# Kernel tuning notes

Hardware: AMD Instinct MI355X
Metric: run time of the kernel (lower is better)

Reference implementation:

```python
import jax, jax.numpy as jnp
import numpy as np

N = 100_000
E = 1_000_000
F_IN = 128
F_OUT = 64
NHOP = 2


def _xavier(k, shape, gain=1.414):
    fan_in, fan_out = shape
    std = gain * np.sqrt(2.0 / (fan_in + fan_out))
    return (jax.random.normal(k, shape) * std).astype(jnp.float32)


def setup_inputs() -> dict:
    key = jax.random.key(0)
    ks = jax.random.split(key, 8)
    x = jax.random.normal(ks[0], (N, F_IN), jnp.float32)
    edge_index = jax.random.randint(ks[1], (2, E), 0, N)
    edge_attr = jax.random.uniform(ks[2], (E,), jnp.float32)
    W0 = _xavier(ks[3], (F_IN, F_OUT))
    W1 = _xavier(ks[4], (F_IN, F_OUT))
    b0 = jnp.zeros((F_OUT,), jnp.float32)
    b1 = jnp.zeros((F_OUT,), jnp.float32)
    fc0 = _xavier(ks[5], (F_OUT, 1))
    fc1 = _xavier(ks[6], (F_OUT, 1))
    bf0 = jnp.zeros((1,), jnp.float32)
    bf1 = jnp.zeros((1,), jnp.float32)
    return dict(x=x, edge_index=edge_index, edge_attr=edge_attr,
                W0=W0, b0=b0, W1=W1, b1=b1,
                fc0=fc0, bf0=bf0, fc1=fc1, bf1=bf1)


def _spmm(row, col, val, v, n):
    # (A v)[r] = sum over edges (r -> c) of val * v[c]
    return jax.ops.segment_sum(val[:, None] * v[col], row, num_segments=n)


def _adaptive_enc(y, fc, bf):
    # NodeAdaptiveEncoder (eval mode): relu(y) + sigmoid(y@fc+bf) * min(y, 0)
    g = jax.nn.sigmoid(y @ fc + bf)  # [N, 1]
    return jnp.where(y < 0, 0.0, y) + g * jnp.where(y > 0, 0.0, y)


def reference(x, edge_index, edge_attr, W0, b0, W1, b1, fc0, bf0, fc1, bf1):
    n = x.shape[0]
    row, col = edge_index[0], edge_index[1]
    ones = jnp.ones((n, 1), x.dtype)
    params = [(W0, b0, fc0, bf0), (W1, b1, fc1, bf1)]
    outs = []
    for hop in range(NHOP):
        W, b, fc, bf = params[hop]
        h = x @ W  # [N, F_OUT]
        # identity attention; row_uniform norm of A^(hop+1) factors as
        # (A^(hop+1) h) / (A^(hop+1) 1) -- exact since spspmm sums duplicates.
        agg, deg = h, ones
        for _ in range(hop + 1):
            agg = _spmm(row, col, edge_attr, agg, n)
            deg = _spmm(row, col, edge_attr, deg, n)
        safe_deg = jnp.where(deg > 0, deg, 1.0)
        y = jnp.where(deg > 0, agg / safe_deg, 0.0)  # NaN mask for empty rows
        y = y + b
        outs.append(_adaptive_enc(y, fc, bf))
    return jnp.concatenate(outs, axis=1)  # [N, NHOP * F_OUT]
```

## Files before the change

### kernel.cpp

```cpp
#include <hip/hip_runtime.h>

#define F_IN 128
#define F_ALL 128
#define F_HOP 64

#define RPB_BITS 9
#define RPB 512
#define KB_MAX 256
#define NBLK_BIN 256
#define ECAP 6144

typedef unsigned int uint;
typedef unsigned short ushort;
typedef __attribute__((ext_vector_type(8))) short short8v;
typedef __attribute__((ext_vector_type(4))) float float4v;

__device__ __forceinline__ uint pack_bf16(float lo, float hi) {
    uint ul = __float_as_uint(lo), uh = __float_as_uint(hi);
    ul += 0x7FFFu + ((ul >> 16) & 1u);
    uh += 0x7FFFu + ((uh >> 16) & 1u);
    return (ul >> 16) | (uh & 0xFFFF0000u);
}
__device__ __forceinline__ float bf_lo(uint h) { return __uint_as_float(h << 16); }
__device__ __forceinline__ float bf_hi(uint h) { return __uint_as_float(h & 0xFFFF0000u); }

__global__ __launch_bounds__(256) void gemm_mfma_kernel(
    const float* __restrict__ x, const float* __restrict__ W0,
    const float* __restrict__ W1, uint* __restrict__ H2, int N) {
    __shared__ ushort Wlds[16384];

    {
        const int t = threadIdx.x;
        #pragma unroll
        for (int i = 0; i < 8; ++i) {
            const int e    = t + 256 * i;
            const int lane = e & 63;
            const int tile = e >> 6;
            const int kt   = tile >> 3;
            const int nt   = tile & 7;
            const int k0   = kt * 32 + (lane >> 4) * 8;
            const int n    = nt * 16 + (lane & 15);
            const float* src = (n < 64) ? (W0 + n) : (W1 + (n - 64));
            float v[8];
            #pragma unroll
            for (int j = 0; j < 8; ++j) v[j] = src[(size_t)(k0 + j) * F_HOP];
            uint4 o;
            o.x = pack_bf16(v[0], v[1]);
            o.y = pack_bf16(v[2], v[3]);
            o.z = pack_bf16(v[4], v[5]);
            o.w = pack_bf16(v[6], v[7]);
            *((uint4*)Wlds + e) = o;
        }
    }
    __syncthreads();

    const int wv   = threadIdx.x >> 6;
    const int lane = threadIdx.x & 63;
    const int rbase = blockIdx.x * 64 + wv * 16;
    if (rbase >= N) return;

    const int m    = lane & 15;
    const int quad = lane >> 4;
    const float* xrow = x + (size_t)(rbase + m) * F_IN + quad * 8;

    float4v acc[8];
    #pragma unroll
    for (int t = 0; t < 8; ++t) acc[t] = (float4v){0.f, 0.f, 0.f, 0.f};

    #pragma unroll
    for (int kt = 0; kt < 4; ++kt) {
        const float4v xa = __builtin_nontemporal_load((const float4v*)(xrow + kt * 32));
        const float4v xb = __builtin_nontemporal_load((const float4v*)(xrow + kt * 32 + 4));
        union { uint4 u; short8v s; } av;
        av.u.x = pack_bf16(xa[0], xa[1]);
        av.u.y = pack_bf16(xa[2], xa[3]);
        av.u.z = pack_bf16(xb[0], xb[1]);
        av.u.w = pack_bf16(xb[2], xb[3]);
        #pragma unroll
        for (int nt = 0; nt < 8; ++nt) {
            union { uint4 u; short8v s; } bv;
            bv.u = *((const uint4*)Wlds + (kt * 8 + nt) * 64 + lane);
            acc[nt] = __builtin_amdgcn_mfma_f32_16x16x32_bf16(av.s, bv.s, acc[nt], 0, 0, 0);
        }
    }

    #pragma unroll
    for (int t = 0; t < 4; ++t) {
        #pragma unroll
        for (int i = 0; i < 4; ++i) {
            const int r = rbase + quad * 4 + i;
            H2[(size_t)r * F_HOP + t * 16 + m] = pack_bf16(acc[t][i], acc[t + 4][i]);
        }
    }
}

__global__ __launch_bounds__(256) void bucket_hist_kernel(
    const int* __restrict__ ei, int* __restrict__ bhist, int E, int K) {
    __shared__ int h[KB_MAX];
    for (int i = threadIdx.x; i < K; i += 256) h[i] = 0;
    __syncthreads();
    const int chunk = (E + NBLK_BIN - 1) / NBLK_BIN;
    const int s = blockIdx.x * chunk;
    const int e = min(s + chunk, E);
    for (int j = s + threadIdx.x; j < e; j += 256)
        atomicAdd(&h[__builtin_nontemporal_load(ei + j) >> RPB_BITS], 1);
    __syncthreads();
    for (int i = threadIdx.x; i < K; i += 256)
        bhist[blockIdx.x * KB_MAX + i] = h[i];
}

__global__ __launch_bounds__(256) void blockscan_kernel(
    int* __restrict__ bhist, int* __restrict__ btot) {
    __shared__ int wsum[4];
    const int b = blockIdx.x;
    const int t = threadIdx.x;
    const int s = bhist[t * KB_MAX + b];
    int v = s;
    #pragma unroll
    for (int d = 1; d < 64; d <<= 1) {
        int u = __shfl_up(v, (unsigned)d, 64);
        if ((t & 63) >= d) v += u;
    }
    if ((t & 63) == 63) wsum[t >> 6] = v;
    __syncthreads();
    int off = 0;
    #pragma unroll
    for (int i = 0; i < 4; ++i) if (i < (t >> 6)) off += wsum[i];
    bhist[t * KB_MAX + b] = off + v - s;
    if (t == 255) btot[b] = off + v;
}

__global__ __launch_bounds__(256) void total_scan_kernel(
    const int* __restrict__ btot, int* __restrict__ bbase,
    int* __restrict__ rowptr, int E, int K, int N) {
    __shared__ int wsum[4];
    const int t = threadIdx.x;
    const int s = (t < K) ? btot[t] : 0;
    int v = s;
    #pragma unroll
    for (int d = 1; d < 64; d <<= 1) {
        int u = __shfl_up(v, (unsigned)d, 64);
        if ((t & 63) >= d) v += u;
    }
    if ((t & 63) == 63) wsum[t >> 6] = v;
    __syncthreads();
    int off = 0;
    #pragma unroll
    for (int i = 0; i < 4; ++i) if (i < (t >> 6)) off += wsum[i];
    const int excl = off + v - s;
    if (t < K) bbase[t] = excl;
    if (t == 0) { bbase[K] = E; rowptr[N] = E; }
}

__global__ __launch_bounds__(256) void bin_kernel(
    const int* __restrict__ ei, const float* __restrict__ ea,
    const int* __restrict__ bloc, const int* __restrict__ bbase,
    int2* __restrict__ gbuf, int E, int K) {
    __shared__ int cur[KB_MAX];
    for (int i = threadIdx.x; i < K; i += 256)
        cur[i] = bbase[i] + bloc[blockIdx.x * KB_MAX + i];
    __syncthreads();
    const int chunk = (E + NBLK_BIN - 1) / NBLK_BIN;
    const int s0 = blockIdx.x * chunk;
    const int e0 = min(s0 + chunk, E);
    for (int j = s0 + threadIdx.x; j < e0; j += 256) {
        const int r = __builtin_nontemporal_load(ei + j);
        const int c = __builtin_nontemporal_load(ei + E + j);
        const int vv = __float_as_int(__builtin_nontemporal_load(ea + j));
        const int b = r >> RPB_BITS;
        const int gp = atomicAdd(&cur[b], 1);
        gbuf[gp] = make_int2(c | ((r & (RPB - 1)) << 17), vv);
    }
}

__global__ __launch_bounds__(1024) void sort_kernel(
    const int* __restrict__ bbase, const int2* __restrict__ gbuf,
    int2* __restrict__ ecv, int* __restrict__ rowptr, int N) {
    __shared__ int2 ebuf[ECAP];
    __shared__ int cnt[RPB];
    __shared__ int wsum[8];
    const int b = blockIdx.x;
    const int t = threadIdx.x;
    const int bstart = bbase[b], bend = bbase[b + 1];
    const int m = bend - bstart;
    const int row0 = b << RPB_BITS;
    if (t < RPB) cnt[t] = 0;
    __syncthreads();
    for (int j = t; j < m; j += 1024) {
        const int2 p = gbuf[bstart + j];
        if (j < ECAP) ebuf[j] = p;
        atomicAdd(&cnt[(p.x >> 17) & (RPB - 1)], 1);
    }
    __syncthreads();
    int v = 0, s = 0;
    if (t < RPB) {
        s = cnt[t];
        v = s;
        #pragma unroll
        for (int d = 1; d < 64; d <<= 1) {
            int u = __shfl_up(v, (unsigned)d, 64);
            if ((t & 63) >= d) v += u;
        }
        if ((t & 63) == 63) wsum[t >> 6] = v;
    }
    __syncthreads();
    if (t < RPB) {
        int off = 0;
        #pragma unroll
        for (int i = 0; i < 8; ++i) if (i < (t >> 6)) off += wsum[i];
        const int excl = off + v - s;
        const int r0 = row0 + t;
        if (r0 < N) rowptr[r0] = bstart + excl;
        cnt[t] = excl;
    }
    __syncthreads();
    for (int j = t; j < m; j += 1024) {
        const int2 p = (j < ECAP) ? ebuf[j] : gbuf[bstart + j];
        const int lr = (p.x >> 17) & (RPB - 1);
        const int pos = atomicAdd(&cnt[lr], 1);
        ecv[bstart + pos] = make_int2(p.x & 0x1FFFF, p.y);
    }
}

__global__ __launch_bounds__(256) void pass1_kernel(
    const int* __restrict__ rowptr, const int2* __restrict__ ecv,
    const uint* __restrict__ H2,
    const float* __restrict__ b0, const float* __restrict__ fc0,
    const float* __restrict__ bf0,
    float* __restrict__ out, ushort* __restrict__ T16,
    float* __restrict__ dg1, int N) {
    const int lane = threadIdx.x & 63;
    const int g    = lane >> 4;
    const int l    = lane & 15;
    const int r = blockIdx.x * 16 + (threadIdx.x >> 6) * 4 + g;
    if (r >= N) return;
    const int f0 = l * 4;
    const uint* __restrict__ H2b = H2 + f0;
    const int jb = rowptr[r], je = rowptr[r + 1];

    float s00 = 0.f, s01 = 0.f, s02 = 0.f, s03 = 0.f;
    float s10 = 0.f, s11 = 0.f, s12 = 0.f, s13 = 0.f;
    float d = 0.f;
    int j = jb;
    for (; j + 4 <= je; j += 4) {
        const int2 e0 = ecv[j], e1 = ecv[j + 1], e2 = ecv[j + 2], e3 = ecv[j + 3];
        const uint4 h0 = *(const uint4*)(H2b + (size_t)e0.x * F_HOP);
        const uint4 h1 = *(const uint4*)(H2b + (size_t)e1.x * F_HOP);
        const uint4 h2 = *(const uint4*)(H2b + (size_t)e2.x * F_HOP);
        const uint4 h3 = *(const uint4*)(H2b + (size_t)e3.x * F_HOP);
        const float v0 = __int_as_float(e0.y), v1 = __int_as_float(e1.y);
        const float v2 = __int_as_float(e2.y), v3 = __int_as_float(e3.y);
        d += (v0 + v1) + (v2 + v3);
        s00 = fmaf(v0, bf_lo(h0.x), s00); s10 = fmaf(v0, bf_hi(h0.x), s10);
        s01 = fmaf(v0, bf_lo(h0.y), s01); s11 = fmaf(v0, bf_hi(h0.y), s11);
        s02 = fmaf(v0, bf_lo(h0.z), s02); s12 = fmaf(v0, bf_hi(h0.z), s12);
        s03 = fmaf(v0, bf_lo(h0.w), s03); s13 = fmaf(v0, bf_hi(h0.w), s13);
        s00 = fmaf(v1, bf_lo(h1.x), s00); s10 = fmaf(v1, bf_hi(h1.x), s10);
        s01 = fmaf(v1, bf_lo(h1.y), s01); s11 = fmaf(v1, bf_hi(h1.y), s11);
        s02 = fmaf(v1, bf_lo(h1.z), s02); s12 = fmaf(v1, bf_hi(h1.z), s12);
        s03 = fmaf(v1, bf_lo(h1.w), s03); s13 = fmaf(v1, bf_hi(h1.w), s13);
        s00 = fmaf(v2, bf_lo(h2.x), s00); s10 = fmaf(v2, bf_hi(h2.x), s10);
        s01 = fmaf(v2, bf_lo(h2.y), s01); s11 = fmaf(v2, bf_hi(h2.y), s11);
        s02 = fmaf(v2, bf_lo(h2.z), s02); s12 = fmaf(v2, bf_hi(h2.z), s12);
        s03 = fmaf(v2, bf_lo(h2.w), s03); s13 = fmaf(v2, bf_hi(h2.w), s13);
        s00 = fmaf(v3, bf_lo(h3.x), s00); s10 = fmaf(v3, bf_hi(h3.x), s10);
        s01 = fmaf(v3, bf_lo(h3.y), s01); s11 = fmaf(v3, bf_hi(h3.y), s11);
        s02 = fmaf(v3, bf_lo(h3.z), s02); s12 = fmaf(v3, bf_hi(h3.z), s12);
        s03 = fmaf(v3, bf_lo(h3.w), s03); s13 = fmaf(v3, bf_hi(h3.w), s13);
    }
    for (; j < je; ++j) {
        const int2 e0 = ecv[j];
        const uint4 h0 = *(const uint4*)(H2b + (size_t)e0.x * F_HOP);
        const float v0 = __int_as_float(e0.y);
        d += v0;
        s00 = fmaf(v0, bf_lo(h0.x), s00); s10 = fmaf(v0, bf_hi(h0.x), s10);
        s01 = fmaf(v0, bf_lo(h0.y), s01); s11 = fmaf(v0, bf_hi(h0.y), s11);
        s02 = fmaf(v0, bf_lo(h0.z), s02); s12 = fmaf(v0, bf_hi(h0.z), s12);
        s03 = fmaf(v0, bf_lo(h0.w), s03); s13 = fmaf(v0, bf_hi(h0.w), s13);
    }

    uint2 tw;
    tw.x = pack_bf16(s10, s11);
    tw.y = pack_bf16(s12, s13);
    *(uint2*)(T16 + (size_t)r * F_HOP + f0) = tw;
    if (l == 0) dg1[r] = d;

    const float inv = (d > 0.f) ? 1.f / d : 0.f;
    const float4 bb = *(const float4*)(b0 + f0);
    const float4 ff = *(const float4*)(fc0 + f0);
    const float y0 = s00 * inv + bb.x;
    const float y1 = s01 * inv + bb.y;
    const float y2 = s02 * inv + bb.z;
    const float y3 = s03 * inv + bb.w;
    float t = y0 * ff.x + y1 * ff.y + y2 * ff.z + y3 * ff.w;
    #pragma unroll
    for (int m = 1; m < 16; m <<= 1) t += __shfl_xor(t, m, 64);
    const float gg = 1.f / (1.f + __expf(-(t + bf0[0])));
    float4v o;
    o[0] = fmaxf(y0, 0.f) + gg * fminf(y0, 0.f);
    o[1] = fmaxf(y1, 0.f) + gg * fminf(y1, 0.f);
    o[2] = fmaxf(y2, 0.f) + gg * fminf(y2, 0.f);
    o[3] = fmaxf(y3, 0.f) + gg * fminf(y3, 0.f);
    __builtin_nontemporal_store(o, (float4v*)(out + (size_t)r * F_ALL + f0));
}

__global__ __launch_bounds__(256) void pass2_kernel(
    const int* __restrict__ rowptr, const int2* __restrict__ ecv,
    const ushort* __restrict__ T16, const float* __restrict__ dg1,
    const float* __restrict__ b1, const float* __restrict__ fc1,
    const float* __restrict__ bf1,
    float* __restrict__ out, int N) {
    const int lane = threadIdx.x & 63;
    const int g    = lane >> 4;
    const int l    = lane & 15;
    const int r = blockIdx.x * 16 + (threadIdx.x >> 6) * 4 + g;
    if (r >= N) return;
    const int f0 = l * 4;
    const ushort* __restrict__ Tb = T16 + f0;
    const int jb = rowptr[r], je = rowptr[r + 1];

    float s0 = 0.f, s1 = 0.f, s2 = 0.f, s3 = 0.f;
    float d2 = 0.f;
    int j = jb;
    for (; j + 4 <= je; j += 4) {
        const int2 e0 = ecv[j], e1 = ecv[j + 1], e2 = ecv[j + 2], e3 = ecv[j + 3];
        const uint2 t0 = *(const uint2*)(Tb + (size_t)e0.x * F_HOP);
        const uint2 t1 = *(const uint2*)(Tb + (size_t)e1.x * F_HOP);
        const uint2 t2 = *(const uint2*)(Tb + (size_t)e2.x * F_HOP);
        const uint2 t3 = *(const uint2*)(Tb + (size_t)e3.x * F_HOP);
        const float g0 = dg1[e0.x], g1 = dg1[e1.x], g2 = dg1[e2.x], g3 = dg1[e3.x];
        const float v0 = __int_as_float(e0.y), v1 = __int_as_float(e1.y);
        const float v2 = __int_as_float(e2.y), v3 = __int_as_float(e3.y);
        d2 = fmaf(v0, g0, d2); d2 = fmaf(v1, g1, d2);
        d2 = fmaf(v2, g2, d2); d2 = fmaf(v3, g3, d2);
        s0 = fmaf(v0, bf_lo(t0.x), s0); s1 = fmaf(v0, bf_hi(t0.x), s1);
        s2 = fmaf(v0, bf_lo(t0.y), s2); s3 = fmaf(v0, bf_hi(t0.y), s3);
        s0 = fmaf(v1, bf_lo(t1.x), s0); s1 = fmaf(v1, bf_hi(t1.x), s1);
        s2 = fmaf(v1, bf_lo(t1.y), s2); s3 = fmaf(v1, bf_hi(t1.y), s3);
        s0 = fmaf(v2, bf_lo(t2.x), s0); s1 = fmaf(v2, bf_hi(t2.x), s1);
        s2 = fmaf(v2, bf_lo(t2.y), s2); s3 = fmaf(v2, bf_hi(t2.y), s3);
        s0 = fmaf(v3, bf_lo(t3.x), s0); s1 = fmaf(v3, bf_hi(t3.x), s1);
        s2 = fmaf(v3, bf_lo(t3.y), s2); s3 = fmaf(v3, bf_hi(t3.y), s3);
    }
    for (; j < je; ++j) {
        const int2 e0 = ecv[j];
        const uint2 t0 = *(const uint2*)(Tb + (size_t)e0.x * F_HOP);
        const float v0 = __int_as_float(e0.y);
        d2 = fmaf(v0, dg1[e0.x], d2);
        s0 = fmaf(v0, bf_lo(t0.x), s0); s1 = fmaf(v0, bf_hi(t0.x), s1);
        s2 = fmaf(v0, bf_lo(t0.y), s2); s3 = fmaf(v0, bf_hi(t0.y), s3);
    }

    const float inv = (d2 > 0.f) ? 1.f / d2 : 0.f;
    const float4 bb = *(const float4*)(b1 + f0);
    const float4 ff = *(const float4*)(fc1 + f0);
    const float y0 = s0 * inv + bb.x;
    const float y1 = s1 * inv + bb.y;
    const float y2 = s2 * inv + bb.z;
    const float y3 = s3 * inv + bb.w;
    float t = y0 * ff.x + y1 * ff.y + y2 * ff.z + y3 * ff.w;
    #pragma unroll
    for (int m = 1; m < 16; m <<= 1) t += __shfl_xor(t, m, 64);
    const float gg = 1.f / (1.f + __expf(-(t + bf1[0])));
    float4v o;
    o[0] = fmaxf(y0, 0.f) + gg * fminf(y0, 0.f);
    o[1] = fmaxf(y1, 0.f) + gg * fminf(y1, 0.f);
    o[2] = fmaxf(y2, 0.f) + gg * fminf(y2, 0.f);
    o[3] = fmaxf(y3, 0.f) + gg * fminf(y3, 0.f);
    __builtin_nontemporal_store(o, (float4v*)(out + (size_t)r * F_ALL + F_HOP + f0));
}

extern "C" void kernel_launch(void* const* d_in, const int* in_sizes, int n_in,
                              void* d_out, int out_size, void* d_ws, size_t ws_size,
                              hipStream_t stream) {
    const float* x   = (const float*)d_in[0];
    const int*   ei  = (const int*)  d_in[1];
    const float* ea  = (const float*)d_in[2];
    const float* W0  = (const float*)d_in[3];
    const float* b0  = (const float*)d_in[4];
    const float* W1  = (const float*)d_in[5];
    const float* b1  = (const float*)d_in[6];
    const float* fc0 = (const float*)d_in[7];
    const float* bf0 = (const float*)d_in[8];
    const float* fc1 = (const float*)d_in[9];
    const float* bf1 = (const float*)d_in[10];
    float* out = (float*)d_out;

    const int N = in_sizes[0] / F_IN;
    const int E = in_sizes[2];
    const int K = (N + RPB - 1) >> RPB_BITS;

    uint*   H2   = (uint*)d_ws;
    ushort* T16  = (ushort*)(H2 + (size_t)N * F_HOP);
    float*  dg1  = (float*)(T16 + (size_t)N * F_HOP);
    int2*   gbuf = (int2*)(dg1 + (size_t)((N + 3) & ~3));
    int2*   ecv  = gbuf + (size_t)E;
    int*    bhist = (int*)(ecv + (size_t)E);
    int*    bbase = bhist + (size_t)NBLK_BIN * KB_MAX;
    int*    btot  = bbase + (KB_MAX + 4);
    int*    rowptr = btot + KB_MAX;

    gemm_mfma_kernel<<<(N + 63) / 64, 256, 0, stream>>>(x, W0, W1, H2, N);

    bucket_hist_kernel<<<NBLK_BIN, 256, 0, stream>>>(ei, bhist, E, K);
    blockscan_kernel<<<K, 256, 0, stream>>>(bhist, btot);
    total_scan_kernel<<<1, 256, 0, stream>>>(btot, bbase, rowptr, E, K, N);
    bin_kernel<<<NBLK_BIN, 256, 0, stream>>>(ei, ea, bhist, bbase, gbuf, E, K);
    sort_kernel<<<K, 1024, 0, stream>>>(bbase, gbuf, ecv, rowptr, N);

    pass1_kernel<<<(N + 15) / 16, 256, 0, stream>>>(
        rowptr, ecv, H2, b0, fc0, bf0, out, T16, dg1, N);

    pass2_kernel<<<(N + 15) / 16, 256, 0, stream>>>(
        rowptr, ecv, T16, dg1, b1, fc1, bf1, out, N);
}
```

Measured before the change: 239.2 us.

## Fuse histogram into GEMM launch, fold total scan into bin/sort, shrink buckets

Runs the edge bucket histogram as extra blocks of the GEMM launch, so both share one grid and can overlap. The separate total-scan kernel is removed: bin_kernel and sort_kernel each recompute the bucket base offsets from btot redundantly. Bucket size drops from 512 to 256 rows, which gives more, smaller sort blocks of 512 threads with a smaller shared edge buffer. This cuts two launches and raises sort parallelism, at the cost of redundant scan work per block and more gbuf spill when a bucket exceeds ECAP.

```diff
diff --git a/kernel.cpp b/kernel.cpp
--- a/kernel.cpp
+++ b/kernel.cpp
@@ -4,11 +4,11 @@
 #define F_ALL 128
 #define F_HOP 64
 
-#define RPB_BITS 9
-#define RPB 512
-#define KB_MAX 256
+#define RPB_BITS 8
+#define RPB 256
+#define KB_MAX 512
 #define NBLK_BIN 256
-#define ECAP 6144
+#define ECAP 3072
 
 typedef unsigned int uint;
 typedef unsigned short ushort;
@@ -24,10 +24,28 @@
 __device__ __forceinline__ float bf_lo(uint h) { return __uint_as_float(h << 16); }
 __device__ __forceinline__ float bf_hi(uint h) { return __uint_as_float(h & 0xFFFF0000u); }
 
-__global__ __launch_bounds__(256) void gemm_mfma_kernel(
+__global__ __launch_bounds__(256) void gemm_hist_kernel(
     const float* __restrict__ x, const float* __restrict__ W0,
-    const float* __restrict__ W1, uint* __restrict__ H2, int N) {
+    const float* __restrict__ W1, uint* __restrict__ H2,
+    const int* __restrict__ ei, int* __restrict__ bhist,
+    int N, int E, int K, int gemmBlocks) {
     __shared__ ushort Wlds[16384];
+
+    if ((int)blockIdx.x >= gemmBlocks) {
+        int* h = (int*)Wlds;
+        const int hb = blockIdx.x - gemmBlocks;
+        for (int i = threadIdx.x; i < K; i += 256) h[i] = 0;
+        __syncthreads();
+        const int chunk = (E + NBLK_BIN - 1) / NBLK_BIN;
+        const int s = hb * chunk;
+        const int e = min(s + chunk, E);
+        for (int j = s + threadIdx.x; j < e; j += 256)
+            atomicAdd(&h[__builtin_nontemporal_load(ei + j) >> RPB_BITS], 1);
+        __syncthreads();
+        for (int i = threadIdx.x; i < K; i += 256)
+            bhist[hb * KB_MAX + i] = h[i];
+        return;
+    }
 
     {
         const int t = threadIdx.x;
@@ -94,23 +112,9 @@
     }
 }
 
-__global__ __launch_bounds__(256) void bucket_hist_kernel(
-    const int* __restrict__ ei, int* __restrict__ bhist, int E, int K) {
-    __shared__ int h[KB_MAX];
-    for (int i = threadIdx.x; i < K; i += 256) h[i] = 0;
-    __syncthreads();
-    const int chunk = (E + NBLK_BIN - 1) / NBLK_BIN;
-    const int s = blockIdx.x * chunk;
-    const int e = min(s + chunk, E);
-    for (int j = s + threadIdx.x; j < e; j += 256)
-        atomicAdd(&h[__builtin_nontemporal_load(ei + j) >> RPB_BITS], 1);
-    __syncthreads();
-    for (int i = threadIdx.x; i < K; i += 256)
-        bhist[blockIdx.x * KB_MAX + i] = h[i];
-}
-
 __global__ __launch_bounds__(256) void blockscan_kernel(
-    int* __restrict__ bhist, int* __restrict__ btot) {
+    int* __restrict__ bhist, int* __restrict__ btot,
+    int* __restrict__ rowptr, int E, int N) {
     __shared__ int wsum[4];
     const int b = blockIdx.x;
     const int t = threadIdx.x;
@@ -128,14 +132,21 @@
     for (int i = 0; i < 4; ++i) if (i < (t >> 6)) off += wsum[i];
     bhist[t * KB_MAX + b] = off + v - s;
     if (t == 255) btot[b] = off + v;
-}
-
-__global__ __launch_bounds__(256) void total_scan_kernel(
-    const int* __restrict__ btot, int* __restrict__ bbase,
-    int* __restrict__ rowptr, int E, int K, int N) {
+    if (b == 0 && t == 0) rowptr[N] = E;
+}
+
+__global__ __launch_bounds__(256) void bin_kernel(
+    const int* __restrict__ ei, const float* __restrict__ ea,
+    const int* __restrict__ bloc, const int* __restrict__ btot,
+    int2* __restrict__ gbuf, int E, int K) {
+    __shared__ int bb[KB_MAX];
+    __shared__ int cur[KB_MAX];
     __shared__ int wsum[4];
     const int t = threadIdx.x;
-    const int s = (t < K) ? btot[t] : 0;
+    const int i0 = 2 * t, i1 = 2 * t + 1;
+    const int c0 = (i0 < K) ? btot[i0] : 0;
+    const int c1 = (i1 < K) ? btot[i1] : 0;
+    const int s = c0 + c1;
     int v = s;
     #pragma unroll
     for (int d = 1; d < 64; d <<= 1) {
@@ -144,26 +155,22 @@
     }
     if ((t & 63) == 63) wsum[t >> 6] = v;
     __syncthreads();
-    int off = 0;
-    #pragma unroll
-    for (int i = 0; i < 4; ++i) if (i < (t >> 6)) off += wsum[i];
-    const int excl = off + v - s;
-    if (t < K) bbase[t] = excl;
-    if (t == 0) { bbase[K] = E; rowptr[N] = E; }
-}
-
-__global__ __launch_bounds__(256) void bin_kernel(
-    const int* __restrict__ ei, const float* __restrict__ ea,
-    const int* __restrict__ bloc, const int* __restrict__ bbase,
-    int2* __restrict__ gbuf, int E, int K) {
-    __shared__ int cur[KB_MAX];
-    for (int i = threadIdx.x; i < K; i += 256)
-        cur[i] = bbase[i] + bloc[blockIdx.x * KB_MAX + i];
+    {
+        int off = 0;
+        #pragma unroll
+        for (int i = 0; i < 4; ++i) if (i < (t >> 6)) off += wsum[i];
+        const int excl = off + v - s;
+        if (i0 < K) bb[i0] = excl;
+        if (i1 < K) bb[i1] = excl + c0;
+    }
+    __syncthreads();
+    for (int i = t; i < K; i += 256)
+        cur[i] = bb[i] + bloc[blockIdx.x * KB_MAX + i];
     __syncthreads();
     const int chunk = (E + NBLK_BIN - 1) / NBLK_BIN;
     const int s0 = blockIdx.x * chunk;
     const int e0 = min(s0 + chunk, E);
-    for (int j = s0 + threadIdx.x; j < e0; j += 256) {
+    for (int j = s0 + t; j < e0; j += 256) {
         const int r = __builtin_nontemporal_load(ei + j);
         const int c = __builtin_nontemporal_load(ei + E + j);
         const int vv = __float_as_int(__builtin_nontemporal_load(ea + j));
@@ -173,48 +180,69 @@
     }
 }
 
-__global__ __launch_bounds__(1024) void sort_kernel(
-    const int* __restrict__ bbase, const int2* __restrict__ gbuf,
-    int2* __restrict__ ecv, int* __restrict__ rowptr, int N) {
+__global__ __launch_bounds__(512) void sort_kernel(
+    const int* __restrict__ btot, const int2* __restrict__ gbuf,
+    int2* __restrict__ ecv, int* __restrict__ rowptr, int E, int K, int N) {
     __shared__ int2 ebuf[ECAP];
     __shared__ int cnt[RPB];
-    __shared__ int wsum[8];
+    __shared__ int bb[KB_MAX + 1];
+    __shared__ int wsum[4];
     const int b = blockIdx.x;
     const int t = threadIdx.x;
-    const int bstart = bbase[b], bend = bbase[b + 1];
+    const int i0 = 2 * t, i1 = 2 * t + 1;
+    const int c0 = (t < 256 && i0 < K) ? btot[i0] : 0;
+    const int c1 = (t < 256 && i1 < K) ? btot[i1] : 0;
+    const int s = c0 + c1;
+    int v = s;
+    #pragma unroll
+    for (int d = 1; d < 64; d <<= 1) {
+        int u = __shfl_up(v, (unsigned)d, 64);
+        if ((t & 63) >= d) v += u;
+    }
+    if (t < 256 && (t & 63) == 63) wsum[t >> 6] = v;
+    if (t < RPB) cnt[t] = 0;
+    __syncthreads();
+    if (t < 256) {
+        int off = 0;
+        #pragma unroll
+        for (int i = 0; i < 4; ++i) if (i < (t >> 6)) off += wsum[i];
+        const int excl = off + v - s;
+        if (i0 < K) bb[i0] = excl;
+        if (i1 < K) bb[i1] = excl + c0;
+    }
+    if (t == 0) bb[K] = E;
+    __syncthreads();
+    const int bstart = bb[b], bend = bb[b + 1];
     const int m = bend - bstart;
     const int row0 = b << RPB_BITS;
-    if (t < RPB) cnt[t] = 0;
-    __syncthreads();
-    for (int j = t; j < m; j += 1024) {
+    for (int j = t; j < m; j += 512) {
         const int2 p = gbuf[bstart + j];
         if (j < ECAP) ebuf[j] = p;
         atomicAdd(&cnt[(p.x >> 17) & (RPB - 1)], 1);
     }
     __syncthreads();
-    int v = 0, s = 0;
-    if (t < RPB) {
-        s = cnt[t];
-        v = s;
-        #pragma unroll
-        for (int d = 1; d < 64; d <<= 1) {
-            int u = __shfl_up(v, (unsigned)d, 64);
-            if ((t & 63) >= d) v += u;
-        }
-        if ((t & 63) == 63) wsum[t >> 6] = v;
-    }
-    __syncthreads();
-    if (t < RPB) {
+    const int s2 = (t < 256) ? cnt[t] : 0;
+    int v2 = s2;
+    #pragma unroll
+    for (int d = 1; d < 64; d <<= 1) {
+        int u = __shfl_up(v2, (unsigned)d, 64);
+        if ((t & 63) >= d) v2 += u;
+    }
+    if (t < 256 && (t & 63) == 63) wsum[t >> 6] = v2;
+    __syncthreads();
+    int excl2 = 0;
+    if (t < 256) {
         int off = 0;
         #pragma unroll
-        for (int i = 0; i < 8; ++i) if (i < (t >> 6)) off += wsum[i];
-        const int excl = off + v - s;
+        for (int i = 0; i < 4; ++i) if (i < (t >> 6)) off += wsum[i];
+        excl2 = off + v2 - s2;
         const int r0 = row0 + t;
-        if (r0 < N) rowptr[r0] = bstart + excl;
-        cnt[t] = excl;
-    }
-    __syncthreads();
-    for (int j = t; j < m; j += 1024) {
+        if (r0 < N) rowptr[r0] = bstart + excl2;
+    }
+    __syncthreads();
+    if (t < 256) cnt[t] = excl2;
+    __syncthreads();
+    for (int j = t; j < m; j += 512) {
         const int2 p = (j < ECAP) ? ebuf[j] : gbuf[bstart + j];
         const int lr = (p.x >> 17) & (RPB - 1);
         const int pos = atomicAdd(&cnt[lr], 1);
@@ -396,17 +424,16 @@
     int2*   gbuf = (int2*)(dg1 + (size_t)((N + 3) & ~3));
     int2*   ecv  = gbuf + (size_t)E;
     int*    bhist = (int*)(ecv + (size_t)E);
-    int*    bbase = bhist + (size_t)NBLK_BIN * KB_MAX;
-    int*    btot  = bbase + (KB_MAX + 4);
-    int*    rowptr = btot + KB_MAX;
-
-    gemm_mfma_kernel<<<(N + 63) / 64, 256, 0, stream>>>(x, W0, W1, H2, N);
-
-    bucket_hist_kernel<<<NBLK_BIN, 256, 0, stream>>>(ei, bhist, E, K);
-    blockscan_kernel<<<K, 256, 0, stream>>>(bhist, btot);
-    total_scan_kernel<<<1, 256, 0, stream>>>(btot, bbase, rowptr, E, K, N);
-    bin_kernel<<<NBLK_BIN, 256, 0, stream>>>(ei, ea, bhist, bbase, gbuf, E, K);
-    sort_kernel<<<K, 1024, 0, stream>>>(bbase, gbuf, ecv, rowptr, N);
+    int*    btot  = bhist + (size_t)NBLK_BIN * KB_MAX;
+    int*    rowptr = btot + (KB_MAX + 4);
+
+    const int gemmBlocks = (N + 63) / 64;
+    gemm_hist_kernel<<<gemmBlocks + NBLK_BIN, 256, 0, stream>>>(
+        x, W0, W1, H2, ei, bhist, N, E, K, gemmBlocks);
+
+    blockscan_kernel<<<K, 256, 0, stream>>>(bhist, btot, rowptr, E, N);
+    bin_kernel<<<NBLK_BIN, 256, 0, stream>>>(ei, ea, bhist, btot, gbuf, E, K);
+    sort_kernel<<<K, 512, 0, stream>>>(btot, gbuf, ecv, rowptr, E, K, N);
 
     pass1_kernel<<<(N + 15) / 16, 256, 0, stream>>>(
         rowptr, ecv, H2, b0, fc0, bf0, out, T16, dg1, N);
```

Measured after the change: 234.9 us. Within noise of the previous version (-1.8%).
